# Optimization experiments

Hardware: AMD Instinct MI355X
Metric: run time of the kernel (lower is better)

The kernel has to match this reference:

```python
import jax, jax.numpy as jnp
import numpy as np

B = 4096; CPG = 2; NPC = 25              # graphs, components/graph, nodes/component
N = B * CPG * NPC; C = B * CPG; E = 409600
IN_CH = 128; HID = 256; L = 3; S = 64; M = 8; NCLS = 2
BN_EPS = 1e-5

def _leaky(x):
    return jax.nn.leaky_relu(x, 0.01)

def _gin_conv(x, src, dst, wa, ba, wb, bb):
    # GINConv with eps=0: mlp(x + sum_{j in N(i)} x_j); messages flow src->dst
    agg = jnp.zeros_like(x).at[dst].add(x[src])
    h = x + agg
    return jax.nn.relu(h @ wa + ba) @ wb + bb

def setup_inputs():
    key = jax.random.key(0)
    ks = jax.random.split(key, 12)
    rn = lambda k, shp: jax.random.normal(k, shp, jnp.float32) * 0.05
    return {
        "x": jax.random.normal(ks[0], (N, IN_CH), jnp.float32),
        "w0a": rn(ks[1], (IN_CH, HID)), "b0a": jnp.zeros((HID,), jnp.float32),
        "w0b": rn(ks[2], (HID, HID)), "b0b": jnp.zeros((HID,), jnp.float32),
        "wra": rn(ks[3], (L - 1, HID, HID)), "bra": jnp.zeros((L - 1, HID), jnp.float32),
        "wrb": rn(ks[4], (L - 1, HID, HID)), "brb": jnp.zeros((L - 1, HID), jnp.float32),
        "Wc": jax.random.uniform(ks[5], (HID, S * M), jnp.float32, -1.0, 1.0),
        "fc1_w": rn(ks[6], (S, 32)), "fc1_b": jnp.zeros((32,), jnp.float32),
        "bn_g": jnp.ones((32,), jnp.float32), "bn_b": jnp.zeros((32,), jnp.float32),
        "fc2_w": rn(ks[7], (32, NCLS)), "fc2_b": jnp.zeros((NCLS,), jnp.float32),
        "edge_index": jax.random.randint(ks[8], (2, E), 0, N, jnp.int32),
        "node2comp": (jnp.arange(N, dtype=jnp.int32) // NPC),
        "comp2graph": (jnp.arange(C, dtype=jnp.int32) // CPG),
        "comp_pos": (jnp.arange(C, dtype=jnp.int32) % CPG),
        "n_graphs": B,
        "max_comps": CPG,
    }

def reference(x, w0a, b0a, w0b, b0b, wra, bra, wrb, brb, Wc, fc1_w, fc1_b, bn_g, bn_b, fc2_w, fc2_b, edge_index, node2comp, comp2graph, comp_pos, n_graphs, max_comps):
    src, dst = edge_index[0], edge_index[1]
    # --- GIN backbone (num_layers convs, ReLU between layers) ---
    h = _gin_conv(x, src, dst, w0a, b0a, w0b, b0b)
    for i in range(wra.shape[0]):
        h = jax.nn.relu(h)
        h = _gin_conv(h, src, dst, wra[i], bra[i], wrb[i], brb[i])
    # --- per-connected-component mean pooling ---
    n_comp = comp2graph.shape[0]
    comp_sum = jax.ops.segment_sum(h, node2comp, num_segments=n_comp)           # [C, d]
    comp_size = jax.ops.segment_sum(jnp.ones((h.shape[0],), h.dtype), node2comp, num_segments=n_comp)
    # torch.mean over the zero-padded cardinality dim divides by the per-graph MAX component size
    graph_maxc = jax.ops.segment_max(comp_size, comp2graph, num_segments=n_graphs)
    comp_mean = comp_sum / graph_maxc[comp2graph][:, None]
    # --- pad components into [B, max_comps, d] ---
    X = jnp.zeros((n_graphs, max_comps, h.shape[1]), h.dtype).at[comp2graph, comp_pos].set(comp_mean)
    # --- set-rep classifier ---
    t = _leaky(jnp.einsum('bcd,dk->bck', X, Wc))                                # [B, maxC, S*M]
    s = fc1_w.shape[0]; m = Wc.shape[1] // s
    t = t.reshape(t.shape[0], t.shape[1], m, s)                                 # view(B, maxC, n_elements, n_hidden_sets)
    t = jnp.max(t, axis=2)
    t = jnp.sum(t, axis=1)                                                      # [B, S]
    t = t @ fc1_w + fc1_b
    mu = jnp.mean(t, axis=0); var = jnp.var(t, axis=0)                          # BN, batch stats (track_running_stats=False)
    t = (t - mu) / jnp.sqrt(var + BN_EPS) * bn_g + bn_b
    t = _leaky(t)
    out = t @ fc2_w + fc2_b
    return jax.nn.log_softmax(out, axis=1)
```

## Files before the change

kernel.cpp:

```cpp
#include <hip/hip_runtime.h>
#include <hip/hip_fp16.h>
#include <math.h>

typedef unsigned short u16;
typedef float f32x4 __attribute__((ext_vector_type(4)));
typedef __bf16 bf16x8 __attribute__((ext_vector_type(8)));

__device__ __forceinline__ float b2f(u16 u) {
    union { unsigned int i; float f; } v; v.i = ((unsigned int)u) << 16; return v.f;
}
__device__ __forceinline__ u16 f2b(float f) {
    union { float f; unsigned int i; } v; v.f = f;
    unsigned int lsb = (v.i >> 16) & 1u;
    return (u16)((v.i + 0x7fffu + lsb) >> 16);
}
__device__ __forceinline__ unsigned int cvtpk(float lo, float hi) {
    unsigned int r;
    asm("v_cvt_pk_bf16_f32 %0, %1, %2" : "=v"(r) : "v"(lo), "v"(hi));
    return r;
}

__global__ __launch_bounds__(256)
void k_scan1(const int* __restrict__ cnt, int* __restrict__ rowptr,
             int* __restrict__ bsum, int N)
{
    __shared__ int s[256];
    int t = threadIdx.x, i = blockIdx.x * 256 + t;
    int v = (i < N) ? cnt[i] : 0;
    s[t] = v;
    __syncthreads();
#pragma unroll
    for (int off = 1; off < 256; off <<= 1) {
        int add = (t >= off) ? s[t - off] : 0;
        __syncthreads();
        s[t] += add;
        __syncthreads();
    }
    if (i < N) rowptr[i] = s[t] - v;
    if (t == 255) bsum[blockIdx.x] = s[255];
}

__global__ __launch_bounds__(256)
void k_scan2(const int* __restrict__ bsum, int* __restrict__ bscan, int nb)
{
    __shared__ int s[256];
    int t = threadIdx.x;
    int g[4], e[4];
    int base = t * 4;
#pragma unroll
    for (int j = 0; j < 4; ++j) g[j] = (base + j < nb) ? bsum[base + j] : 0;
    e[0] = 0; e[1] = g[0]; e[2] = g[0] + g[1]; e[3] = g[0] + g[1] + g[2];
    int tsum = e[3] + g[3];
    s[t] = tsum;
    __syncthreads();
#pragma unroll
    for (int off = 1; off < 256; off <<= 1) {
        int add = (t >= off) ? s[t - off] : 0;
        __syncthreads();
        s[t] += add;
        __syncthreads();
    }
    int texcl = s[t] - tsum;
#pragma unroll
    for (int j = 0; j < 4; ++j)
        if (base + j < nb) bscan[base + j] = texcl + e[j];
}

__global__ __launch_bounds__(256)
void k_scan3(int* __restrict__ rowptr, const int* __restrict__ bscan,
             int* __restrict__ cursor, int N)
{
    int i = blockIdx.x * 256 + threadIdx.x;
    if (i >= N) return;
    int r = rowptr[i] + bscan[i >> 8];
    rowptr[i] = r;
    cursor[i] = r;
}

__global__ __launch_bounds__(256)
void k_fill(const int* __restrict__ src, const int* __restrict__ dst,
            int* __restrict__ cursor, int* __restrict__ col, int E)
{
    int e = blockIdx.x * 256 + threadIdx.x;
    if (e >= E) return;
    int pos = atomicAdd(&cursor[dst[e]], 1);
    col[pos] = src[e];
}

__global__ __launch_bounds__(256)
void k_setup(const float* __restrict__ w0a, const float* __restrict__ w0b,
             const float* __restrict__ wra, const float* __restrict__ wrb,
             const float* __restrict__ Wc,  u16* __restrict__ wt,
             const int* __restrict__ dst, int* __restrict__ cnt, int E)
{
    int t = blockIdx.x * 256 + threadIdx.x;
    if (t < E) atomicAdd(&cnt[dst[t]], 1);

    const float* in; u16* out; int K, N, l;
    if      (t < 32768)  { in = w0a;          out = wt;          K = 128; N = 256; l = t; }
    else if (t < 98304)  { in = w0b;          out = wt + 65536;  K = 256; N = 256; l = t - 32768; }
    else if (t < 163840) { in = wra;          out = wt + 131072; K = 256; N = 256; l = t - 98304; }
    else if (t < 229376) { in = wra + 65536;  out = wt + 196608; K = 256; N = 256; l = t - 163840; }
    else if (t < 294912) { in = wrb;          out = wt + 262144; K = 256; N = 256; l = t - 229376; }
    else if (t < 360448) { in = wrb + 65536;  out = wt + 327680; K = 256; N = 256; l = t - 294912; }
    else if (t < 491520) { in = Wc;           out = wt + 393216; K = 256; N = 512; l = t - 360448; }
    else return;
    out[l] = f2b(in[(l % K) * N + l / K]);
}

#define CCAP 512

template<int K, bool RELU, bool F32SRC>
__global__ __launch_bounds__(512, 6)
void k_gin(const void* __restrict__ hsrc,
           const int* __restrict__ cnt, const int* __restrict__ rowptr,
           const int* __restrict__ col,
           const u16* __restrict__ WaT, const float* __restrict__ ba,
           const u16* __restrict__ WbT, const float* __restrict__ bb,
           u16* __restrict__ Hout, int Ntot, int Etot)
{
    __shared__ u16 AH[64 * 256];
    __shared__ int colLDS[CCAP];

    const int tid = threadIdx.x, lane = tid & 63, wave = tid >> 6;
    const int bm0 = blockIdx.x * 64;
    const int cw0 = wave * 32;
    const int l15 = lane & 15, lq = lane >> 4;

    const int rp0 = rowptr[bm0];
    const int rpE = (bm0 + 64 < Ntot) ? rowptr[bm0 + 64] : Etot;
    const int total = rpE - rp0;
    for (int i = tid; i < total && i < CCAP; i += 512) colLDS[i] = col[rp0 + i];

    bf16x8 bpre0 = *(const bf16x8*)(WaT + (size_t)(cw0 + l15) * K + lq * 8);
    bf16x8 bpre1 = *(const bf16x8*)(WaT + (size_t)(cw0 + 16 + l15) * K + lq * 8);
    __syncthreads();

    {
        constexpr int NSEG = K / 8;
        const int gr = tid >> 3, gseg = tid & 7;
        const int node = bm0 + gr;
        const int nn = cnt[node], rp = rowptr[node];
        const int jbase = rp - rp0;
        const int nIt = nn + 1;

        float acc[NSEG];
#pragma unroll
        for (int i = 0; i < NSEG; ++i) acc[i] = 0.f;

        if (F32SRC) {
            const float4* bp = (const float4*)hsrc;
            const int stride = K / 4, off = gseg * (NSEG / 4);
            const float4* p = bp + (size_t)node * stride + off;
            float4 a0 = p[0], a1 = p[1];
            for (int t = 0; t < nIt; ++t) {
                float4 b0 = p[2], b1 = p[3];
                int tn = (t + 1 < nIt) ? t + 1 : t;
                int jl = jbase + tn - 1;
                int idxN = (tn == 0) ? node : ((jl < CCAP) ? colLDS[jl] : col[rp + tn - 1]);
                const float4* q = bp + (size_t)idxN * stride + off;
                float4 n0 = q[0], n1 = q[1];
                if (RELU) {
                    acc[0] += fmaxf(a0.x,0.f); acc[1] += fmaxf(a0.y,0.f); acc[2] += fmaxf(a0.z,0.f); acc[3] += fmaxf(a0.w,0.f);
                    acc[4] += fmaxf(a1.x,0.f); acc[5] += fmaxf(a1.y,0.f); acc[6] += fmaxf(a1.z,0.f); acc[7] += fmaxf(a1.w,0.f);
                    acc[8] += fmaxf(b0.x,0.f); acc[9] += fmaxf(b0.y,0.f); acc[10]+= fmaxf(b0.z,0.f); acc[11]+= fmaxf(b0.w,0.f);
                    acc[12]+= fmaxf(b1.x,0.f); acc[13]+= fmaxf(b1.y,0.f); acc[14]+= fmaxf(b1.z,0.f); acc[15]+= fmaxf(b1.w,0.f);
                } else {
                    acc[0] += a0.x; acc[1] += a0.y; acc[2] += a0.z; acc[3] += a0.w;
                    acc[4] += a1.x; acc[5] += a1.y; acc[6] += a1.z; acc[7] += a1.w;
                    acc[8] += b0.x; acc[9] += b0.y; acc[10]+= b0.z; acc[11]+= b0.w;
                    acc[12]+= b1.x; acc[13]+= b1.y; acc[14]+= b1.z; acc[15]+= b1.w;
                }
                a0 = n0; a1 = n1; p = q;
            }
        } else {
            const uint4* bp = (const uint4*)hsrc;
            const int stride = K / 8, off = gseg * (NSEG / 8);
            const uint4* p = bp + (size_t)node * stride + off;
            uint4 a0 = p[0], a1 = p[1];
            for (int t = 0; t < nIt; ++t) {
                uint4 b0 = p[2], b1 = p[3];
                int tn = (t + 1 < nIt) ? t + 1 : t;
                int jl = jbase + tn - 1;
                int idxN = (tn == 0) ? node : ((jl < CCAP) ? colLDS[jl] : col[rp + tn - 1]);
                const uint4* q = bp + (size_t)idxN * stride + off;
                uint4 n0 = q[0], n1 = q[1];
                u16 vs[32] __attribute__((aligned(16)));
                *(uint4*)(vs + 0)  = a0; *(uint4*)(vs + 8)  = a1;
                *(uint4*)(vs + 16) = b0; *(uint4*)(vs + 24) = b1;
#pragma unroll
                for (int i2 = 0; i2 < 32; ++i2) {
                    float x = b2f(vs[i2]);
                    acc[i2] += RELU ? fmaxf(x, 0.f) : x;
                }
                a0 = n0; a1 = n1; p = q;
            }
        }

        const int k0 = gseg * NSEG;
        constexpr int NKC = NSEG / 8;
#pragma unroll
        for (int cc = 0; cc < NKC; ++cc) {
            const int k = k0 + cc * 8;
            const int s  = (k >> 5) * 256 + (gr >> 4) * 64 + ((k >> 3) & 3) * 16 + (gr & 15);
            const int sp = s ^ ((k >> 5) & 7);
            uint4 pk;
            pk.x = cvtpk(acc[cc * 8 + 0], acc[cc * 8 + 1]);
            pk.y = cvtpk(acc[cc * 8 + 2], acc[cc * 8 + 3]);
            pk.z = cvtpk(acc[cc * 8 + 4], acc[cc * 8 + 5]);
            pk.w = cvtpk(acc[cc * 8 + 6], acc[cc * 8 + 7]);
            *(uint4*)(AH + sp * 8) = pk;
        }
    }
    __syncthreads();

    constexpr int NK1 = K / 32;
    f32x4 acc1[4][2];
#pragma unroll
    for (int r = 0; r < 4; ++r)
#pragma unroll
        for (int c = 0; c < 2; ++c) acc1[r][c] = (f32x4){0.f, 0.f, 0.f, 0.f};

#pragma unroll
    for (int kb = 0; kb < NK1; ++kb) {
        bf16x8 a[4], b[2];
        if (kb == 0) { b[0] = bpre0; b[1] = bpre1; }
        else {
#pragma unroll
            for (int c = 0; c < 2; ++c)
                b[c] = *(const bf16x8*)(WaT + (size_t)(cw0 + c * 16 + l15) * K + kb * 32 + lq * 8);
        }
#pragma unroll
        for (int r = 0; r < 4; ++r)
            a[r] = *(const bf16x8*)&AH[(kb * 256 + r * 64 + (lane ^ (kb & 7))) * 8];
        __builtin_amdgcn_s_setprio(1);
#pragma unroll
        for (int r = 0; r < 4; ++r)
#pragma unroll
            for (int c = 0; c < 2; ++c)
                acc1[r][c] = __builtin_amdgcn_mfma_f32_16x16x32_bf16(b[c], a[r], acc1[r][c], 0, 0, 0);
        __builtin_amdgcn_s_setprio(0);
    }
    __syncthreads();

#pragma unroll
    for (int c = 0; c < 2; ++c) {
        const int n0 = cw0 + c * 16 + lq * 4;
        const float4 bv = *(const float4*)(ba + n0);
        const int sbase = (n0 >> 5) * 256 + ((n0 >> 3) & 3) * 16 + l15;
        const int sx = (n0 >> 5) & 7;
#pragma unroll
        for (int r = 0; r < 4; ++r) {
            float v0 = fmaxf(acc1[r][c][0] + bv.x, 0.f);
            float v1 = fmaxf(acc1[r][c][1] + bv.y, 0.f);
            float v2 = fmaxf(acc1[r][c][2] + bv.z, 0.f);
            float v3 = fmaxf(acc1[r][c][3] + bv.w, 0.f);
            uint2 pk; pk.x = cvtpk(v0, v1); pk.y = cvtpk(v2, v3);
            const int sp = (sbase + r * 64) ^ sx;
            *(uint2*)(AH + sp * 8 + (n0 & 7)) = pk;
        }
    }
    __syncthreads();

    f32x4 acc2[4][2];
#pragma unroll
    for (int r = 0; r < 4; ++r)
#pragma unroll
        for (int c = 0; c < 2; ++c) acc2[r][c] = (f32x4){0.f, 0.f, 0.f, 0.f};

#pragma unroll
    for (int kb = 0; kb < 8; ++kb) {
        bf16x8 a[4], b[2];
#pragma unroll
        for (int c = 0; c < 2; ++c)
            b[c] = *(const bf16x8*)(WbT + (size_t)(cw0 + c * 16 + l15) * 256 + kb * 32 + lq * 8);
#pragma unroll
        for (int r = 0; r < 4; ++r)
            a[r] = *(const bf16x8*)&AH[(kb * 256 + r * 64 + (lane ^ (kb & 7))) * 8];
        __builtin_amdgcn_s_setprio(1);
#pragma unroll
        for (int r = 0; r < 4; ++r)
#pragma unroll
            for (int c = 0; c < 2; ++c)
                acc2[r][c] = __builtin_amdgcn_mfma_f32_16x16x32_bf16(b[c], a[r], acc2[r][c], 0, 0, 0);
        __builtin_amdgcn_s_setprio(0);
    }
#pragma unroll
    for (int c = 0; c < 2; ++c) {
        const int n0 = cw0 + c * 16 + lq * 4;
        const float4 bv = *(const float4*)(bb + n0);
#pragma unroll
        for (int r = 0; r < 4; ++r) {
            const int node = bm0 + r * 16 + l15;
            uint2 pk;
            pk.x = cvtpk(acc2[r][c][0] + bv.x, acc2[r][c][1] + bv.y);
            pk.y = cvtpk(acc2[r][c][2] + bv.z, acc2[r][c][3] + bv.w);
            *(uint2*)(Hout + (size_t)node * 256 + n0) = pk;
        }
    }
}

__global__ __launch_bounds__(256)
void k_lin(const u16* __restrict__ A, const u16* __restrict__ WT,
           float* __restrict__ C)
{
    __shared__ u16 As[64 * 40];
    __shared__ u16 Bs[256 * 40];
    const int tid = threadIdx.x, lane = tid & 63, wave = tid >> 6;
    const int bm0 = blockIdx.x * 64, bn0 = blockIdx.y * 256;
    const int fm = lane & 15, fk = (lane >> 4) * 8;
    const int lc = lane & 15, lr = (lane >> 4) * 4;
    const int cw0 = wave * 64;
    const int sr = tid >> 2, sc = tid & 3;

    f32x4 acc[4][4];
#pragma unroll
    for (int r = 0; r < 4; ++r)
#pragma unroll
        for (int c = 0; c < 4; ++c) acc[r][c] = (f32x4){0.f, 0.f, 0.f, 0.f};

    for (int k0 = 0; k0 < 256; k0 += 32) {
        *(uint4*)&As[sr * 40 + sc * 8] =
            *(const uint4*)(A + (size_t)(bm0 + sr) * 256 + k0 + sc * 8);
        {
            const uint4* wp = (const uint4*)(WT + (size_t)(bn0 + tid) * 256 + k0);
#pragma unroll
            for (int c = 0; c < 4; ++c)
                *(uint4*)&Bs[tid * 40 + c * 8] = wp[c];
        }
        __syncthreads();
        bf16x8 a[4], b[4];
#pragma unroll
        for (int r = 0; r < 4; ++r) a[r] = *(const bf16x8*)&As[(r * 16 + fm) * 40 + fk];
#pragma unroll
        for (int c = 0; c < 4; ++c) b[c] = *(const bf16x8*)&Bs[(cw0 + c * 16 + fm) * 40 + fk];
#pragma unroll
        for (int r = 0; r < 4; ++r)
#pragma unroll
            for (int c = 0; c < 4; ++c)
                acc[r][c] = __builtin_amdgcn_mfma_f32_16x16x32_bf16(a[r], b[c], acc[r][c], 0, 0, 0);
        __syncthreads();
    }
#pragma unroll
    for (int c = 0; c < 4; ++c) {
        const int col = bn0 + cw0 + c * 16 + lc;
#pragma unroll
        for (int r = 0; r < 4; ++r)
#pragma unroll
            for (int i = 0; i < 4; ++i) {
                float v = acc[r][c][i];
                v = (v >= 0.f) ? v : 0.01f * v;
                C[(size_t)(bm0 + r * 16 + lr + i) * 512 + col] = v;
            }
    }
}

__global__ void k_pool(const u16* __restrict__ H, u16* __restrict__ Xc)
{
    int c = blockIdx.x, f = threadIdx.x;
    const u16* p = H + (size_t)c * 25 * 256 + f;
    float s = 0.f;
#pragma unroll
    for (int j = 0; j < 25; ++j) s += b2f(p[j * 256]);
    Xc[(size_t)c * 256 + f] = f2b(s / 25.0f);
}

__global__ void k_setpool(const float* __restrict__ T, float* __restrict__ Tp)
{
    int tid = blockIdx.x * 256 + threadIdx.x;
    int b = tid >> 6, s = tid & 63;
    float acc = 0.f;
#pragma unroll
    for (int c = 0; c < 2; ++c) {
        const float* row = T + ((size_t)(b * 2 + c)) * 512 + s;
        float mx = row[0];
#pragma unroll
        for (int m = 1; m < 8; ++m) mx = fmaxf(mx, row[m * 64]);
        acc += mx;
    }
    Tp[tid] = acc;
}

__global__ void k_fc1(const float* __restrict__ Tp, const float* __restrict__ w,
                      const float* __restrict__ b, float* __restrict__ T1)
{
    int tid = blockIdx.x * 256 + threadIdx.x;
    int bb = tid >> 5, j = tid & 31;
    float s = b[j];
#pragma unroll
    for (int k = 0; k < 64; ++k) s += Tp[bb * 64 + k] * w[k * 32 + j];
    T1[tid] = s;
}

__global__ void k_bnstats(const float* __restrict__ T1, float* __restrict__ stats)
{
    __shared__ float r1[256], r2[256];
    const int j = blockIdx.x, t = threadIdx.x;
    float s = 0.f, ss = 0.f;
    for (int b = t; b < 4096; b += 256) {
        float v = T1[b * 32 + j];
        s += v; ss += v * v;
    }
    r1[t] = s; r2[t] = ss;
    __syncthreads();
    for (int off = 128; off > 0; off >>= 1) {
        if (t < off) { r1[t] += r1[t + off]; r2[t] += r2[t + off]; }
        __syncthreads();
    }
    if (t == 0) {
        float mu  = r1[0] * (1.f / 4096.f);
        float var = r2[0] * (1.f / 4096.f) - mu * mu;
        stats[j]      = mu;
        stats[32 + j] = 1.f / sqrtf(var + 1e-5f);
    }
}

__global__ void k_head(const float* __restrict__ T1, const float* __restrict__ stats,
                       const float* __restrict__ g, const float* __restrict__ bb,
                       const float* __restrict__ w2, const float* __restrict__ b2,
                       float* __restrict__ out)
{
    const int b = blockIdx.x * 256 + threadIdx.x;
    float l0 = b2[0], l1 = b2[1];
#pragma unroll
    for (int j = 0; j < 32; ++j) {
        float v = (T1[b * 32 + j] - stats[j]) * stats[32 + j] * g[j] + bb[j];
        v = (v >= 0.f) ? v : 0.01f * v;
        l0 += v * w2[j * 2];
        l1 += v * w2[j * 2 + 1];
    }
    float mx  = fmaxf(l0, l1);
    float lse = mx + logf(expf(l0 - mx) + expf(l1 - mx));
    out[b * 2]     = l0 - lse;
    out[b * 2 + 1] = l1 - lse;
}

extern "C" void kernel_launch(void* const* d_in, const int* in_sizes, int n_in,
                              void* d_out, int out_size, void* d_ws, size_t ws_size,
                              hipStream_t stream)
{
    (void)n_in; (void)out_size; (void)ws_size;
    constexpr int NN = 204800, NCOMP = 8192, NGRAPH = 4096;

    const float* x    = (const float*)d_in[0];
    const float* w0a  = (const float*)d_in[1];
    const float* b0a  = (const float*)d_in[2];
    const float* w0b  = (const float*)d_in[3];
    const float* b0b  = (const float*)d_in[4];
    const float* wra  = (const float*)d_in[5];
    const float* bra  = (const float*)d_in[6];
    const float* wrb  = (const float*)d_in[7];
    const float* brb  = (const float*)d_in[8];
    const float* Wc   = (const float*)d_in[9];
    const float* f1w  = (const float*)d_in[10];
    const float* f1b  = (const float*)d_in[11];
    const float* bng  = (const float*)d_in[12];
    const float* bnb  = (const float*)d_in[13];
    const float* f2w  = (const float*)d_in[14];
    const float* f2bb = (const float*)d_in[15];
    const int* ei   = (const int*)d_in[16];
    const int  E    = in_sizes[16] / 2;
    const int* src  = ei;
    const int* dst  = ei + E;

    char* ws = (char*)d_ws;
    u16*    H1  = (u16*)ws;
    u16*    H0  = (u16*)(ws + (size_t)104857600);
    u16*    wt  = (u16*)(ws + (size_t)209715200);
    u16 *WT0 = wt, *WT1 = wt + 65536, *WT2 = wt + 131072, *WT3 = wt + 196608,
        *WT4 = wt + 262144, *WT5 = wt + 327680, *WT6 = wt + 393216;
    char* csr = ws + (size_t)210763776;
    int* cnt    = (int*)csr;
    int* rowptr = (int*)(csr + 819200);
    int* cursor = (int*)(csr + 1638400);
    int* col    = (int*)(csr + 2457600);
    int* bsum   = (int*)(csr + 4096000);
    int* bscan  = (int*)(csr + 4100096);
    u16*   Xc    = (u16*)ws;
    float* Tfull = (float*)(ws + (size_t)16777216);
    float* Tp    = (float*)(ws + (size_t)33554432);
    float* T1    = (float*)(ws + (size_t)41943040);
    float* stats = (float*)(ws + (size_t)46137344);

    const dim3 blk(256);
    const dim3 blk512(512);
    const int NB = NN / 256;

    hipMemsetAsync(cnt, 0, NN * 4, stream);
    k_setup<<<1920, blk, 0, stream>>>(w0a, w0b, wra, wrb, Wc, wt, dst, cnt, E);
    k_scan1<<<NB, blk, 0, stream>>>(cnt, rowptr, bsum, NN);
    k_scan2<<<1, blk, 0, stream>>>(bsum, bscan, NB);
    k_scan3<<<NB, blk, 0, stream>>>(rowptr, bscan, cursor, NN);
    k_fill<<<(E + 255) / 256, blk, 0, stream>>>(src, dst, cursor, col, E);

    k_gin<128, false, true><<<NN / 64, blk512, 0, stream>>>(
        x, cnt, rowptr, col, WT0, b0a, WT1, b0b, H0, NN, E);
    k_gin<256, true, false><<<NN / 64, blk512, 0, stream>>>(
        H0, cnt, rowptr, col, WT2, bra, WT4, brb, H1, NN, E);
    k_gin<256, true, false><<<NN / 64, blk512, 0, stream>>>(
        H1, cnt, rowptr, col, WT3, bra + 256, WT5, brb + 256, H0, NN, E);

    k_pool<<<NCOMP, blk, 0, stream>>>(H0, Xc);
    k_lin<<<dim3(NCOMP / 64, 2), blk, 0, stream>>>(Xc, WT6, Tfull);
    k_setpool<<<(NGRAPH * 64) / 256, blk, 0, stream>>>(Tfull, Tp);
    k_fc1<<<(NGRAPH * 32) / 256, blk, 0, stream>>>(Tp, f1w, f1b, T1);
    k_bnstats<<<32, blk, 0, stream>>>(T1, stats);
    k_head<<<NGRAPH / 256, blk, 0, stream>>>(T1, stats, bng, bnb, f2w, f2bb, (float*)d_out);
}
```

Measured before the change: 723.0 us.

## Swap MFMA operand order in GIN kernel and fuse setpool with fc1

The GIN kernel now passes the MFMA operands in swapped order, so each lane holds four consecutive nodes of one feature column instead of four consecutive features. Its epilogues change to match, writing scalar bf16 values to shared memory and global memory in place of packed 8-byte stores. Separately, the set max/sum pooling and fc1 are merged into one kernel that passes its intermediate through shared memory, removing one launch and the Tp round trip. The scalar 2-byte global stores with a 512-byte stride across the four rows may coalesce worse than the earlier vector stores.

After: 687.6 us. -4.9%, faster.

```diff
diff --git a/kernel.cpp b/kernel.cpp
--- a/kernel.cpp
+++ b/kernel.cpp
@@ -124,6 +124,7 @@
 
     const int tid = threadIdx.x, lane = tid & 63, wave = tid >> 6;
     const int bm0 = blockIdx.x * 64;
+    const int lc = lane & 15, lr = (lane >> 4) * 4;
     const int cw0 = wave * 32;
     const int l15 = lane & 15, lq = lane >> 4;
 
@@ -238,27 +239,24 @@
         for (int r = 0; r < 4; ++r)
 #pragma unroll
             for (int c = 0; c < 2; ++c)
-                acc1[r][c] = __builtin_amdgcn_mfma_f32_16x16x32_bf16(b[c], a[r], acc1[r][c], 0, 0, 0);
+                acc1[r][c] = __builtin_amdgcn_mfma_f32_16x16x32_bf16(a[r], b[c], acc1[r][c], 0, 0, 0);
         __builtin_amdgcn_s_setprio(0);
     }
     __syncthreads();
 
 #pragma unroll
     for (int c = 0; c < 2; ++c) {
-        const int n0 = cw0 + c * 16 + lq * 4;
-        const float4 bv = *(const float4*)(ba + n0);
-        const int sbase = (n0 >> 5) * 256 + ((n0 >> 3) & 3) * 16 + l15;
-        const int sx = (n0 >> 5) & 7;
-#pragma unroll
-        for (int r = 0; r < 4; ++r) {
-            float v0 = fmaxf(acc1[r][c][0] + bv.x, 0.f);
-            float v1 = fmaxf(acc1[r][c][1] + bv.y, 0.f);
-            float v2 = fmaxf(acc1[r][c][2] + bv.z, 0.f);
-            float v3 = fmaxf(acc1[r][c][3] + bv.w, 0.f);
-            uint2 pk; pk.x = cvtpk(v0, v1); pk.y = cvtpk(v2, v3);
-            const int sp = (sbase + r * 64) ^ sx;
-            *(uint2*)(AH + sp * 8 + (n0 & 7)) = pk;
-        }
+        const int n = cw0 + c * 16 + lc;
+        const float bv = ba[n];
+        const int nb = (n >> 5) * 256 + ((n >> 3) & 3) * 16;
+        const int sx = (n >> 5) & 7;
+#pragma unroll
+        for (int r = 0; r < 4; ++r)
+#pragma unroll
+            for (int i = 0; i < 4; ++i) {
+                const int sp = (nb + r * 64 + lr + i) ^ sx;
+                AH[sp * 8 + (n & 7)] = f2b(fmaxf(acc1[r][c][i] + bv, 0.f));
+            }
     }
     __syncthreads();
 
@@ -282,21 +280,18 @@
         for (int r = 0; r < 4; ++r)
 #pragma unroll
             for (int c = 0; c < 2; ++c)
-                acc2[r][c] = __builtin_amdgcn_mfma_f32_16x16x32_bf16(b[c], a[r], acc2[r][c], 0, 0, 0);
+                acc2[r][c] = __builtin_amdgcn_mfma_f32_16x16x32_bf16(a[r], b[c], acc2[r][c], 0, 0, 0);
         __builtin_amdgcn_s_setprio(0);
     }
 #pragma unroll
     for (int c = 0; c < 2; ++c) {
-        const int n0 = cw0 + c * 16 + lq * 4;
-        const float4 bv = *(const float4*)(bb + n0);
-#pragma unroll
-        for (int r = 0; r < 4; ++r) {
-            const int node = bm0 + r * 16 + l15;
-            uint2 pk;
-            pk.x = cvtpk(acc2[r][c][0] + bv.x, acc2[r][c][1] + bv.y);
-            pk.y = cvtpk(acc2[r][c][2] + bv.z, acc2[r][c][3] + bv.w);
-            *(uint2*)(Hout + (size_t)node * 256 + n0) = pk;
-        }
+        const int n = cw0 + c * 16 + lc;
+        const float bv = bb[n];
+#pragma unroll
+        for (int r = 0; r < 4; ++r)
+#pragma unroll
+            for (int i = 0; i < 4; ++i)
+                Hout[(size_t)(bm0 + r * 16 + lr + i) * 256 + n] = f2b(acc2[r][c][i] + bv);
     }
 }
 
@@ -365,31 +360,32 @@
     Xc[(size_t)c * 256 + f] = f2b(s / 25.0f);
 }
 
-__global__ void k_setpool(const float* __restrict__ T, float* __restrict__ Tp)
-{
-    int tid = blockIdx.x * 256 + threadIdx.x;
-    int b = tid >> 6, s = tid & 63;
-    float acc = 0.f;
-#pragma unroll
-    for (int c = 0; c < 2; ++c) {
-        const float* row = T + ((size_t)(b * 2 + c)) * 512 + s;
-        float mx = row[0];
-#pragma unroll
-        for (int m = 1; m < 8; ++m) mx = fmaxf(mx, row[m * 64]);
-        acc += mx;
-    }
-    Tp[tid] = acc;
-}
-
-__global__ void k_fc1(const float* __restrict__ Tp, const float* __restrict__ w,
-                      const float* __restrict__ b, float* __restrict__ T1)
-{
-    int tid = blockIdx.x * 256 + threadIdx.x;
-    int bb = tid >> 5, j = tid & 31;
-    float s = b[j];
-#pragma unroll
-    for (int k = 0; k < 64; ++k) s += Tp[bb * 64 + k] * w[k * 32 + j];
-    T1[tid] = s;
+__global__ __launch_bounds__(256)
+void k_sf(const float* __restrict__ T, const float* __restrict__ w,
+          const float* __restrict__ b, float* __restrict__ T1)
+{
+    __shared__ float tp[8][64];
+    const int gl = threadIdx.x >> 5, j = threadIdx.x & 31;
+    const int g = blockIdx.x * 8 + gl;
+#pragma unroll
+    for (int h = 0; h < 2; ++h) {
+        const int s = j + h * 32;
+        float acc = 0.f;
+#pragma unroll
+        for (int c = 0; c < 2; ++c) {
+            const float* row = T + ((size_t)(g * 2 + c)) * 512 + s;
+            float mx = row[0];
+#pragma unroll
+            for (int m = 1; m < 8; ++m) mx = fmaxf(mx, row[m * 64]);
+            acc += mx;
+        }
+        tp[gl][s] = acc;
+    }
+    __syncthreads();
+    float sum = b[j];
+#pragma unroll
+    for (int k = 0; k < 64; ++k) sum += tp[gl][k] * w[k * 32 + j];
+    T1[g * 32 + j] = sum;
 }
 
 __global__ void k_bnstats(const float* __restrict__ T1, float* __restrict__ stats)
@@ -478,7 +474,6 @@
     int* bscan  = (int*)(csr + 4100096);
     u16*   Xc    = (u16*)ws;
     float* Tfull = (float*)(ws + (size_t)16777216);
-    float* Tp    = (float*)(ws + (size_t)33554432);
     float* T1    = (float*)(ws + (size_t)41943040);
     float* stats = (float*)(ws + (size_t)46137344);
 
@@ -502,8 +497,7 @@
 
     k_pool<<<NCOMP, blk, 0, stream>>>(H0, Xc);
     k_lin<<<dim3(NCOMP / 64, 2), blk, 0, stream>>>(Xc, WT6, Tfull);
-    k_setpool<<<(NGRAPH * 64) / 256, blk, 0, stream>>>(Tfull, Tp);
-    k_fc1<<<(NGRAPH * 32) / 256, blk, 0, stream>>>(Tp, f1w, f1b, T1);
+    k_sf<<<NGRAPH / 8, blk, 0, stream>>>(Tfull, f1w, f1b, T1);
     k_bnstats<<<32, blk, 0, stream>>>(T1, stats);
     k_head<<<NGRAPH / 256, blk, 0, stream>>>(T1, stats, bng, bnb, f2w, f2bb, (float*)d_out);
 }
```
